# Kernel tuning notes

Hardware: AMD Instinct MI355X
Metric: run time of the kernel (lower is better)

Reference implementation:

```python
import jax, jax.numpy as jnp
import numpy as np

K = 3          # kernel size
PAD = 1        # padding
# deformable conv v2: offset conv (2*K*K ch), modulator conv (K*K ch, 2*sigmoid), main 3x3 conv, ReLU


def _conv2d(x, w, b):
    y = jax.lax.conv_general_dilated(x, w, (1, 1), ((PAD, PAD), (PAD, PAD)),
                                     dimension_numbers=('NCHW', 'OIHW', 'NCHW'))
    return y + b[None, :, None, None]


def _bilinear_gather(x, py, px):
    # x: [B,C,H,W]; py/px: [B,K2,H,W] float sample coords; zero outside image.
    B, C, H, W = x.shape
    y0 = jnp.floor(py)
    x0 = jnp.floor(px)
    wy1 = py - y0
    wx1 = px - x0
    wy0 = 1.0 - wy1
    wx0 = 1.0 - wx1
    xf = x.reshape(B, C, H * W)

    def gather(yi, xi):
        valid = (yi >= 0) & (yi <= H - 1) & (xi >= 0) & (xi <= W - 1)
        yc = jnp.clip(yi, 0, H - 1).astype(jnp.int32)
        xc = jnp.clip(xi, 0, W - 1).astype(jnp.int32)
        idx = (yc * W + xc).reshape(B, -1)                      # [B, K2*H*W]
        v = jax.vmap(lambda xb, ib: xb[:, ib])(xf, idx)         # [B, C, K2*H*W]
        v = v.reshape(B, C, *yi.shape[1:])                      # [B, C, K2, H, W]
        return v * valid[:, None].astype(x.dtype)

    return (gather(y0, x0) * (wy0 * wx0)[:, None]
            + gather(y0, x0 + 1) * (wy0 * wx1)[:, None]
            + gather(y0 + 1, x0) * (wy1 * wx0)[:, None]
            + gather(y0 + 1, x0 + 1) * (wy1 * wx1)[:, None])


def _deform_conv(data, w, b, w_off, b_off, w_mod, b_mod):
    B, Cin, H, W = data.shape
    off = _conv2d(data, w_off, b_off)                           # [B, 2*K2, H, W]
    mask = 2.0 * jax.nn.sigmoid(_conv2d(data, w_mod, b_mod))    # [B, K2, H, W]
    off = off.reshape(B, K * K, 2, H, W)                        # (dy, dx) per tap
    dy, dx = off[:, :, 0], off[:, :, 1]
    ki, kj = jnp.meshgrid(jnp.arange(K), jnp.arange(K), indexing='ij')
    ki = ki.reshape(-1).astype(data.dtype)
    kj = kj.reshape(-1).astype(data.dtype)
    hs = jnp.arange(H, dtype=data.dtype)
    ws = jnp.arange(W, dtype=data.dtype)
    py = hs[None, None, :, None] - PAD + ki[None, :, None, None] + dy
    px = ws[None, None, None, :] - PAD + kj[None, :, None, None] + dx
    sampled = _bilinear_gather(data, py, px)                    # [B, Cin, K2, H, W]
    sampled = sampled * mask[:, None]
    out = jnp.einsum('bckhw,ock->bohw', sampled, w.reshape(w.shape[0], Cin, K * K))
    return out + b[None, :, None, None]


def setup_inputs() -> dict:
    key = jax.random.key(0)
    ks = jax.random.split(key, 7)
    B, Cin, Cout, H, W = 8, 64, 64, 128, 128
    fan = Cin * K * K
    return {
        'data': jax.random.normal(ks[0], (B, Cin, H, W), jnp.float32),
        'w': jax.random.normal(ks[1], (Cout, Cin, K, K), jnp.float32) / np.sqrt(fan),
        'b': jax.random.normal(ks[2], (Cout,), jnp.float32) * 0.01,
        'w_off': jax.random.normal(ks[3], (2 * K * K, Cin, K, K), jnp.float32) * (0.1 / np.sqrt(fan)),
        'b_off': jnp.zeros((2 * K * K,), jnp.float32),
        'w_mod': jax.random.normal(ks[4], (K * K, Cin, K, K), jnp.float32) * (0.1 / np.sqrt(fan)),
        'b_mod': jnp.zeros((K * K,), jnp.float32),
    }


def reference(data, w, b, w_off, b_off, w_mod, b_mod):
    return jax.nn.relu(_deform_conv(data, w, b, w_off, b_off, w_mod, b_mod))
```

## Files before the change

### kernel.cpp

```cpp
#include <hip/hip_runtime.h>
#include <hip/hip_bf16.h>
#include <cstdint>


typedef __attribute__((ext_vector_type(8))) short short8;
typedef __attribute__((ext_vector_type(4))) float floatx4;
typedef __attribute__((ext_vector_type(2))) float floatx2;

__device__ __forceinline__ unsigned short f2bf(float x) {
    unsigned int u = __float_as_uint(x);
    u += 0x7fffu + ((u >> 16) & 1u);
    return (unsigned short)(u >> 16);
}
__device__ __forceinline__ unsigned int pack2bf(float lo, float hi) {
    unsigned int ul = __float_as_uint(lo); ul += 0x7fffu + ((ul >> 16) & 1u);
    unsigned int uh = __float_as_uint(hi); uh += 0x7fffu + ((uh >> 16) & 1u);
    return __builtin_amdgcn_perm(uh, ul, 0x07060302u);
}
__device__ __forceinline__ floatx2 up2(unsigned int u) {
    floatx2 r;
    r.x = __uint_as_float(u << 16);
    r.y = __uint_as_float(u & 0xffff0000u);
    return r;
}
__device__ __forceinline__ unsigned int blend2pk(unsigned int a, unsigned int b,
                                                 unsigned int c, unsigned int d,
                                                 float4 fw) {
    floatx2 s = up2(a) * fw.x;
    s += up2(b) * fw.y;
    s += up2(c) * fw.z;
    s += up2(d) * fw.w;
    __hip_bfloat162 h = __float22bfloat162_rn(make_float2(s.x, s.y));
    return *(unsigned int*)&h;
}

#define OFF_DATAT 0u
#define OFF_OFFP  16777216u
#define OFF_WM    30932992u
#define OFF_W27   31006720u
#define OFF_B27   31043584u

__global__ void pack_weights_k(const float* __restrict__ w,
                               const float* __restrict__ w_off,
                               const float* __restrict__ w_mod,
                               const float* __restrict__ b_off,
                               const float* __restrict__ b_mod,
                               unsigned short* __restrict__ wpackM,
                               unsigned short* __restrict__ wpack27,
                               float* __restrict__ bias27) {
    int t = blockIdx.x * 256 + threadIdx.x;
    if (t < 64 * 576) {
        int o = t / 576, kk = t % 576;
        int k = kk >> 6, c = kk & 63;
        wpackM[t] = f2bf(w[(o * 64 + c) * 9 + k]);
        return;
    }
    t -= 64 * 576;
    if (t < 32 * 576) {
        int o = t / 576, kk = t % 576;
        int k = kk >> 6, c = kk & 63;
        float v = 0.f;
        if (o < 18)      v = w_off[(o * 64 + c) * 9 + k];
        else if (o < 27) v = w_mod[((o - 18) * 64 + c) * 9 + k];
        wpack27[t] = f2bf(v);
        if (kk == 0) bias27[o] = (o < 18) ? b_off[o] : (o < 27 ? b_mod[o - 18] : 0.f);
    }
}

__global__ __launch_bounds__(256) void transpose_k(const float* __restrict__ x,
                                                   unsigned short* __restrict__ xt) {
    __shared__ float tile[64][65];
    int blk  = blockIdx.x;
    int b    = blk >> 8;
    int pos0 = (blk & 255) << 6;
    int lane = threadIdx.x & 63;
    int g    = threadIdx.x >> 6;
    for (int c = g; c < 64; c += 4)
        tile[c][lane] = x[(((b << 6) + c) << 14) + pos0 + lane];
    __syncthreads();
    int c2 = lane & 31;
    for (int i = g; i < 32; i += 4) {
        int pr = (i << 1) + (lane >> 5);
        unsigned int d = pack2bf(tile[c2 << 1][pr], tile[(c2 << 1) + 1][pr]);
        *(unsigned int*)&xt[((size_t)((b << 14) + pos0 + pr) << 6) + (c2 << 1)] = d;
    }
}

__global__ __launch_bounds__(256) void conv27_k(const unsigned short* __restrict__ xt,
                                                const unsigned short* __restrict__ wpack27,
                                                const float* __restrict__ bias27,
                                                float* __restrict__ offP) {
    __shared__ unsigned short tile[4][66][72];
    int blk   = blockIdx.x;
    int b     = blk >> 7;
    int patch = blk & 127;
    int m     = patch >> 1;
    int h     = patch & 1;
    int tid   = threadIdx.x;
    int lane  = tid & 63, wv = tid >> 6;
    int r = lane & 15, q = lane >> 4;

    const unsigned short* xb = xt + ((size_t)b << 20);

    {
        int g = tid >> 3, j = tid & 7;
        #pragma unroll
        for (int rr = 0; rr < 4; ++rr) {
            int sy = (m << 1) + rr - 1;
            #pragma unroll
            for (int ci = 0; ci < 3; ++ci) {
                int col = g + (ci << 5);
                if (col < 66) {
                    int sx = (h << 6) + col - 1;
                    uint4 v = {0u, 0u, 0u, 0u};
                    if (sy >= 0 && sy < 128 && sx >= 0 && sx < 128)
                        v = *(const uint4*)&xb[(size_t)(((sy << 7) + sx) << 6) + (j << 3)];
                    *(uint4*)&tile[rr][col][j << 3] = v;
                }
            }
        }
    }
    __syncthreads();

    floatx4 acc[4] = {};
    #pragma unroll
    for (int k = 0; k < 9; ++k) {
        int ki = k / 3, kj = k % 3;
        #pragma unroll
        for (int ch = 0; ch < 2; ++ch) {
            short8 a0 = *(const short8*)&wpack27[(r)      * 576 + (k << 6) + (ch << 5) + (q << 3)];
            short8 a1 = *(const short8*)&wpack27[(16 + r) * 576 + (k << 6) + (ch << 5) + (q << 3)];
            #pragma unroll
            for (int tr = 0; tr < 2; ++tr) {
                short8 bfrag = *(const short8*)&tile[tr + ki][(wv << 4) + r + kj][(ch << 5) + (q << 3)];
                acc[0 + tr] = __builtin_amdgcn_mfma_f32_16x16x32_bf16(a0, bfrag, acc[0 + tr], 0, 0, 0);
                acc[2 + tr] = __builtin_amdgcn_mfma_f32_16x16x32_bf16(a1, bfrag, acc[2 + tr], 0, 0, 0);
            }
        }
    }

    #pragma unroll
    for (int s = 0; s < 2; ++s) {
        #pragma unroll
        for (int tr = 0; tr < 2; ++tr) {
            #pragma unroll
            for (int reg = 0; reg < 4; ++reg) {
                int oc = (s << 4) + (q << 2) + reg;
                if (oc >= 27) continue;
                int pos = (((m << 1) + tr) << 7) + (h << 6) + (wv << 4) + r;
                float v = acc[(s << 1) + tr][reg] + bias27[oc];
                int kk, comp;
                if (oc < 18) { kk = oc >> 1; comp = oc & 1; }
                else         { kk = oc - 18; comp = 2; v = 2.f / (1.f + __expf(-v)); }
                offP[(size_t)(((b * 9 + kk) * 3 + comp) << 14) + pos] = v;
            }
        }
    }
}

__global__ __launch_bounds__(256) void deform_main_k(const unsigned short* __restrict__ xt,
                                                     const unsigned short* __restrict__ wpackM,
                                                     const float* __restrict__ offP,
                                                     const float* __restrict__ bias,
                                                     float* __restrict__ out) {
    __shared__ int4   pOff[576];
    __shared__ float4 pW[576];
    __shared__ unsigned short samp[2][64][72];
    int blk  = blockIdx.x;
    int b    = blk >> 8;
    int pos0 = (blk & 255) << 6;
    int tid  = threadIdx.x;
    int lane = tid & 63, wv = tid >> 6;
    int r = lane & 15, q = lane >> 4;
    int pg = lane >> 3;
    int j8 = lane & 7;

    const char* xbb = (const char*)(xt + ((size_t)b << 20));

    for (int e = tid; e < 576; e += 256) {
        int k = e >> 6, p = e & 63;
        int pos = pos0 + p;
        const float* offk = offP + ((size_t)((b * 9 + k) * 3) << 14);
        float dy = offk[pos];
        float dx = offk[16384 + pos];
        float m  = offk[32768 + pos];
        float py = (float)(pos >> 7) + (float)(k / 3 - 1) + dy;
        float px = (float)(pos & 127) + (float)(k % 3 - 1) + dx;
        float y0f = floorf(py), x0f = floorf(px);
        int y0 = (int)y0f, x0 = (int)x0f;
        float wy1 = py - y0f, wx1 = px - x0f;
        float wy0 = 1.f - wy1, wx0 = 1.f - wx1;
        bool vy0 = (y0 >= 0) && (y0 < 128);
        bool vy1 = (y0 >= -1) && (y0 < 127);
        bool vx0 = (x0 >= 0) && (x0 < 128);
        bool vx1 = (x0 >= -1) && (x0 < 127);
        float w00 = (vy0 && vx0) ? m * wy0 * wx0 : 0.f;
        float w01 = (vy0 && vx1) ? m * wy0 * wx1 : 0.f;
        float w10 = (vy1 && vx0) ? m * wy1 * wx0 : 0.f;
        float w11 = (vy1 && vx1) ? m * wy1 * wx1 : 0.f;
        int y0c = min(max(y0, 0), 127), y1c = min(max(y0 + 1, 0), 127);
        int x0c = min(max(x0, 0), 127), x1c = min(max(x0 + 1, 0), 127);
        pOff[e] = make_int4(((y0c << 7) + x0c) << 7, ((y0c << 7) + x1c) << 7,
                            ((y1c << 7) + x0c) << 7, ((y1c << 7) + x1c) << 7);
        pW[e] = make_float4(w00, w01, w10, w11);
    }
    __syncthreads();

    floatx4 acc[4] = {};
    const char* xp = xbb + (j8 << 4);
    const unsigned short* wrow = wpackM + ((wv << 4) + r) * 576 + (q << 3);

    uint4  c00[2], c01[2], c10[2], c11[2];
    float4 cw[2];
    short8 afC[2], afN[2];

    auto issue = [&](int k) {
        #pragma unroll
        for (int i = 0; i < 2; ++i) {
            int e  = (k << 6) + (wv << 4) + (i << 3) + pg;
            int4   io = pOff[e];
            cw[i]  = pW[e];
            c00[i] = *(const uint4*)(xp + io.x);
            c01[i] = *(const uint4*)(xp + io.y);
            c10[i] = *(const uint4*)(xp + io.z);
            c11[i] = *(const uint4*)(xp + io.w);
        }
    };
    auto blendStore = [&](int buf) {
        #pragma unroll
        for (int i = 0; i < 2; ++i) {
            int p = (wv << 4) + (i << 3) + pg;
            uint4 o4;
            o4.x = blend2pk(c00[i].x, c01[i].x, c10[i].x, c11[i].x, cw[i]);
            o4.y = blend2pk(c00[i].y, c01[i].y, c10[i].y, c11[i].y, cw[i]);
            o4.z = blend2pk(c00[i].z, c01[i].z, c10[i].z, c11[i].z, cw[i]);
            o4.w = blend2pk(c00[i].w, c01[i].w, c10[i].w, c11[i].w, cw[i]);
            *(uint4*)&samp[buf][p][j8 << 3] = o4;
        }
    };

    issue(0);
    afC[0] = *(const short8*)&wrow[0];
    afC[1] = *(const short8*)&wrow[32];
    blendStore(0);

    for (int k = 0; k < 9; ++k) {
        if (k < 8) {
            issue(k + 1);
            afN[0] = *(const short8*)&wrow[((k + 1) << 6)];
            afN[1] = *(const short8*)&wrow[((k + 1) << 6) + 32];
        }
        __syncthreads();
        #pragma unroll
        for (int ch = 0; ch < 2; ++ch) {
            #pragma unroll
            for (int nt = 0; nt < 4; ++nt) {
                short8 bfrag = *(const short8*)&samp[k & 1][(nt << 4) + r][(ch << 5) + (q << 3)];
                acc[nt] = __builtin_amdgcn_mfma_f32_16x16x32_bf16(afC[ch], bfrag, acc[nt], 0, 0, 0);
            }
        }
        if (k < 8) {
            blendStore((k + 1) & 1);
            afC[0] = afN[0];
            afC[1] = afN[1];
        }
    }

    #pragma unroll
    for (int nt = 0; nt < 4; ++nt) {
        #pragma unroll
        for (int reg = 0; reg < 4; ++reg) {
            int oc  = (wv << 4) + (q << 2) + reg;
            int pos = pos0 + (nt << 4) + r;
            float v = acc[nt][reg] + bias[oc];
            out[(size_t)(((b << 6) + oc) << 14) + pos] = fmaxf(v, 0.f);
        }
    }
}

extern "C" void kernel_launch(void* const* d_in, const int* in_sizes, int n_in,
                              void* d_out, int out_size, void* d_ws, size_t ws_size,
                              hipStream_t stream) {
    const float* data  = (const float*)d_in[0];
    const float* w     = (const float*)d_in[1];
    const float* bias  = (const float*)d_in[2];
    const float* w_off = (const float*)d_in[3];
    const float* b_off = (const float*)d_in[4];
    const float* w_mod = (const float*)d_in[5];
    const float* b_mod = (const float*)d_in[6];
    float* out = (float*)d_out;

    char* ws = (char*)d_ws;
    unsigned short* dataT   = (unsigned short*)(ws + OFF_DATAT);
    float*          offP    = (float*)(ws + OFF_OFFP);
    unsigned short* wpackM  = (unsigned short*)(ws + OFF_WM);
    unsigned short* wpack27 = (unsigned short*)(ws + OFF_W27);
    float*          bias27  = (float*)(ws + OFF_B27);

    pack_weights_k<<<216, 256, 0, stream>>>(w, w_off, w_mod, b_off, b_mod,
                                            wpackM, wpack27, bias27);
    transpose_k<<<2048, 256, 0, stream>>>(data, dataT);
    conv27_k<<<1024, 256, 0, stream>>>(dataT, wpack27, bias27, offP);
    deform_main_k<<<2048, 256, 0, stream>>>(dataT, wpackM, offP, bias, out);
}
```

Baseline: 165.1 us.

## Fuse offset/mask conv into deformable main kernel and merge prep kernels

The offset/modulator 3x3 conv is now computed inside the deformable-conv kernel for each 64-pixel row segment. A 3-row halo is loaded into shared memory and the result is kept in a shared buffer that overlays the halo through a union, so the offP intermediate no longer makes a round trip through global memory. The transpose and weight-packing kernels are merged into a single launch, cutting launches from four to two. The trade-off is that each block reloads a 3-row halo, and the extra shared-memory use and barriers in the fused kernel may lower occupancy.

```diff
diff --git a/kernel.cpp b/kernel.cpp
--- a/kernel.cpp
+++ b/kernel.cpp
@@ -35,20 +35,35 @@
 }
 
 #define OFF_DATAT 0u
-#define OFF_OFFP  16777216u
-#define OFF_WM    30932992u
-#define OFF_W27   31006720u
-#define OFF_B27   31043584u
-
-__global__ void pack_weights_k(const float* __restrict__ w,
-                               const float* __restrict__ w_off,
-                               const float* __restrict__ w_mod,
-                               const float* __restrict__ b_off,
-                               const float* __restrict__ b_mod,
-                               unsigned short* __restrict__ wpackM,
-                               unsigned short* __restrict__ wpack27,
-                               float* __restrict__ bias27) {
-    int t = blockIdx.x * 256 + threadIdx.x;
+#define OFF_WM    16777216u
+#define OFF_W27   16850944u
+
+__global__ __launch_bounds__(256) void prep_k(const float* __restrict__ x,
+                                              unsigned short* __restrict__ xt,
+                                              const float* __restrict__ w,
+                                              const float* __restrict__ w_off,
+                                              const float* __restrict__ w_mod,
+                                              unsigned short* __restrict__ wpackM,
+                                              unsigned short* __restrict__ wpack27) {
+    __shared__ float tile[64][65];
+    int blk = blockIdx.x;
+    if (blk < 2048) {
+        int b    = blk >> 8;
+        int pos0 = (blk & 255) << 6;
+        int lane = threadIdx.x & 63;
+        int g    = threadIdx.x >> 6;
+        for (int c = g; c < 64; c += 4)
+            tile[c][lane] = x[(((b << 6) + c) << 14) + pos0 + lane];
+        __syncthreads();
+        int c2 = lane & 31;
+        for (int i = g; i < 32; i += 4) {
+            int pr = (i << 1) + (lane >> 5);
+            unsigned int d = pack2bf(tile[c2 << 1][pr], tile[(c2 << 1) + 1][pr]);
+            *(unsigned int*)&xt[((size_t)((b << 14) + pos0 + pr) << 6) + (c2 << 1)] = d;
+        }
+        return;
+    }
+    int t = (blk - 2048) * 256 + threadIdx.x;
     if (t < 64 * 576) {
         int o = t / 576, kk = t % 576;
         int k = kk >> 6, c = kk & 63;
@@ -63,50 +78,45 @@
         if (o < 18)      v = w_off[(o * 64 + c) * 9 + k];
         else if (o < 27) v = w_mod[((o - 18) * 64 + c) * 9 + k];
         wpack27[t] = f2bf(v);
-        if (kk == 0) bias27[o] = (o < 18) ? b_off[o] : (o < 27 ? b_mod[o - 18] : 0.f);
-    }
-}
-
-__global__ __launch_bounds__(256) void transpose_k(const float* __restrict__ x,
-                                                   unsigned short* __restrict__ xt) {
-    __shared__ float tile[64][65];
+    }
+}
+
+__global__ __launch_bounds__(256) void deform_fused_k(const unsigned short* __restrict__ xt,
+                                                      const unsigned short* __restrict__ wpackM,
+                                                      const unsigned short* __restrict__ wpack27,
+                                                      const float* __restrict__ b_off,
+                                                      const float* __restrict__ b_mod,
+                                                      const float* __restrict__ bias,
+                                                      float* __restrict__ out) {
+    __shared__ union {
+        unsigned short halo[3][66][72];
+        struct {
+            float convOut[32][64];
+            unsigned short samp[2][64][72];
+        } s2;
+    } U;
+    __shared__ int4   pOff[576];
+    __shared__ float4 pW[576];
+
     int blk  = blockIdx.x;
     int b    = blk >> 8;
     int pos0 = (blk & 255) << 6;
-    int lane = threadIdx.x & 63;
-    int g    = threadIdx.x >> 6;
-    for (int c = g; c < 64; c += 4)
-        tile[c][lane] = x[(((b << 6) + c) << 14) + pos0 + lane];
-    __syncthreads();
-    int c2 = lane & 31;
-    for (int i = g; i < 32; i += 4) {
-        int pr = (i << 1) + (lane >> 5);
-        unsigned int d = pack2bf(tile[c2 << 1][pr], tile[(c2 << 1) + 1][pr]);
-        *(unsigned int*)&xt[((size_t)((b << 14) + pos0 + pr) << 6) + (c2 << 1)] = d;
-    }
-}
-
-__global__ __launch_bounds__(256) void conv27_k(const unsigned short* __restrict__ xt,
-                                                const unsigned short* __restrict__ wpack27,
-                                                const float* __restrict__ bias27,
-                                                float* __restrict__ offP) {
-    __shared__ unsigned short tile[4][66][72];
-    int blk   = blockIdx.x;
-    int b     = blk >> 7;
-    int patch = blk & 127;
-    int m     = patch >> 1;
-    int h     = patch & 1;
-    int tid   = threadIdx.x;
-    int lane  = tid & 63, wv = tid >> 6;
+    int y    = (blk & 255) >> 1;
+    int h    = blk & 1;
+    int tid  = threadIdx.x;
+    int lane = tid & 63, wv = tid >> 6;
     int r = lane & 15, q = lane >> 4;
-
-    const unsigned short* xb = xt + ((size_t)b << 20);
+    int pg = lane >> 3;
+    int j8 = lane & 7;
+
+    const unsigned short* xb  = xt + ((size_t)b << 20);
+    const char*           xbb = (const char*)xb;
 
     {
         int g = tid >> 3, j = tid & 7;
         #pragma unroll
-        for (int rr = 0; rr < 4; ++rr) {
-            int sy = (m << 1) + rr - 1;
+        for (int rr = 0; rr < 3; ++rr) {
+            int sy = y + rr - 1;
             #pragma unroll
             for (int ci = 0; ci < 3; ++ci) {
                 int col = g + (ci << 5);
@@ -115,75 +125,50 @@
                     uint4 v = {0u, 0u, 0u, 0u};
                     if (sy >= 0 && sy < 128 && sx >= 0 && sx < 128)
                         v = *(const uint4*)&xb[(size_t)(((sy << 7) + sx) << 6) + (j << 3)];
-                    *(uint4*)&tile[rr][col][j << 3] = v;
+                    *(uint4*)&U.halo[rr][col][j << 3] = v;
                 }
             }
         }
     }
     __syncthreads();
 
-    floatx4 acc[4] = {};
-    #pragma unroll
-    for (int k = 0; k < 9; ++k) {
-        int ki = k / 3, kj = k % 3;
-        #pragma unroll
-        for (int ch = 0; ch < 2; ++ch) {
-            short8 a0 = *(const short8*)&wpack27[(r)      * 576 + (k << 6) + (ch << 5) + (q << 3)];
-            short8 a1 = *(const short8*)&wpack27[(16 + r) * 576 + (k << 6) + (ch << 5) + (q << 3)];
-            #pragma unroll
-            for (int tr = 0; tr < 2; ++tr) {
-                short8 bfrag = *(const short8*)&tile[tr + ki][(wv << 4) + r + kj][(ch << 5) + (q << 3)];
-                acc[0 + tr] = __builtin_amdgcn_mfma_f32_16x16x32_bf16(a0, bfrag, acc[0 + tr], 0, 0, 0);
-                acc[2 + tr] = __builtin_amdgcn_mfma_f32_16x16x32_bf16(a1, bfrag, acc[2 + tr], 0, 0, 0);
-            }
-        }
-    }
-
-    #pragma unroll
-    for (int s = 0; s < 2; ++s) {
-        #pragma unroll
-        for (int tr = 0; tr < 2; ++tr) {
+    {
+        int i_oc = wv >> 1, j_pos = wv & 1;
+        floatx4 acc2[2] = {};
+        #pragma unroll
+        for (int k = 0; k < 9; ++k) {
+            int ki = k / 3, kj = k % 3;
+            #pragma unroll
+            for (int ch = 0; ch < 2; ++ch) {
+                short8 a = *(const short8*)&wpack27[((i_oc << 4) + r) * 576 + (k << 6) + (ch << 5) + (q << 3)];
+                #pragma unroll
+                for (int nt = 0; nt < 2; ++nt) {
+                    int col = (j_pos << 5) + (nt << 4) + r + kj;
+                    short8 bf = *(const short8*)&U.halo[ki][col][(ch << 5) + (q << 3)];
+                    acc2[nt] = __builtin_amdgcn_mfma_f32_16x16x32_bf16(a, bf, acc2[nt], 0, 0, 0);
+                }
+            }
+        }
+        __syncthreads();
+        #pragma unroll
+        for (int nt = 0; nt < 2; ++nt) {
             #pragma unroll
             for (int reg = 0; reg < 4; ++reg) {
-                int oc = (s << 4) + (q << 2) + reg;
-                if (oc >= 27) continue;
-                int pos = (((m << 1) + tr) << 7) + (h << 6) + (wv << 4) + r;
-                float v = acc[(s << 1) + tr][reg] + bias27[oc];
-                int kk, comp;
-                if (oc < 18) { kk = oc >> 1; comp = oc & 1; }
-                else         { kk = oc - 18; comp = 2; v = 2.f / (1.f + __expf(-v)); }
-                offP[(size_t)(((b * 9 + kk) * 3 + comp) << 14) + pos] = v;
-            }
-        }
-    }
-}
-
-__global__ __launch_bounds__(256) void deform_main_k(const unsigned short* __restrict__ xt,
-                                                     const unsigned short* __restrict__ wpackM,
-                                                     const float* __restrict__ offP,
-                                                     const float* __restrict__ bias,
-                                                     float* __restrict__ out) {
-    __shared__ int4   pOff[576];
-    __shared__ float4 pW[576];
-    __shared__ unsigned short samp[2][64][72];
-    int blk  = blockIdx.x;
-    int b    = blk >> 8;
-    int pos0 = (blk & 255) << 6;
-    int tid  = threadIdx.x;
-    int lane = tid & 63, wv = tid >> 6;
-    int r = lane & 15, q = lane >> 4;
-    int pg = lane >> 3;
-    int j8 = lane & 7;
-
-    const char* xbb = (const char*)(xt + ((size_t)b << 20));
+                int oc  = (i_oc << 4) + (q << 2) + reg;
+                int pl  = (j_pos << 5) + (nt << 4) + r;
+                U.s2.convOut[oc][pl] = acc2[nt][reg];
+            }
+        }
+    }
+    __syncthreads();
 
     for (int e = tid; e < 576; e += 256) {
         int k = e >> 6, p = e & 63;
         int pos = pos0 + p;
-        const float* offk = offP + ((size_t)((b * 9 + k) * 3) << 14);
-        float dy = offk[pos];
-        float dx = offk[16384 + pos];
-        float m  = offk[32768 + pos];
+        float dy = U.s2.convOut[(k << 1)][p]     + b_off[(k << 1)];
+        float dx = U.s2.convOut[(k << 1) + 1][p] + b_off[(k << 1) + 1];
+        float mm = U.s2.convOut[18 + k][p]       + b_mod[k];
+        float m  = 2.f / (1.f + __expf(-mm));
         float py = (float)(pos >> 7) + (float)(k / 3 - 1) + dy;
         float px = (float)(pos & 127) + (float)(k % 3 - 1) + dx;
         float y0f = floorf(py), x0f = floorf(px);
@@ -235,7 +220,7 @@
             o4.y = blend2pk(c00[i].y, c01[i].y, c10[i].y, c11[i].y, cw[i]);
             o4.z = blend2pk(c00[i].z, c01[i].z, c10[i].z, c11[i].z, cw[i]);
             o4.w = blend2pk(c00[i].w, c01[i].w, c10[i].w, c11[i].w, cw[i]);
-            *(uint4*)&samp[buf][p][j8 << 3] = o4;
+            *(uint4*)&U.s2.samp[buf][p][j8 << 3] = o4;
         }
     };
 
@@ -255,7 +240,7 @@
         for (int ch = 0; ch < 2; ++ch) {
             #pragma unroll
             for (int nt = 0; nt < 4; ++nt) {
-                short8 bfrag = *(const short8*)&samp[k & 1][(nt << 4) + r][(ch << 5) + (q << 3)];
+                short8 bfrag = *(const short8*)&U.s2.samp[k & 1][(nt << 4) + r][(ch << 5) + (q << 3)];
                 acc[nt] = __builtin_amdgcn_mfma_f32_16x16x32_bf16(afC[ch], bfrag, acc[nt], 0, 0, 0);
             }
         }
@@ -292,14 +277,10 @@
 
     char* ws = (char*)d_ws;
     unsigned short* dataT   = (unsigned short*)(ws + OFF_DATAT);
-    float*          offP    = (float*)(ws + OFF_OFFP);
     unsigned short* wpackM  = (unsigned short*)(ws + OFF_WM);
     unsigned short* wpack27 = (unsigned short*)(ws + OFF_W27);
-    float*          bias27  = (float*)(ws + OFF_B27);
-
-    pack_weights_k<<<216, 256, 0, stream>>>(w, w_off, w_mod, b_off, b_mod,
-                                            wpackM, wpack27, bias27);
-    transpose_k<<<2048, 256, 0, stream>>>(data, dataT);
-    conv27_k<<<1024, 256, 0, stream>>>(dataT, wpack27, bias27, offP);
-    deform_main_k<<<2048, 256, 0, stream>>>(dataT, wpackM, offP, bias, out);
-}
+
+    prep_k<<<2264, 256, 0, stream>>>(data, dataT, w, w_off, w_mod, wpackM, wpack27);
+    deform_fused_k<<<2048, 256, 0, stream>>>(dataT, wpackM, wpack27,
+                                             b_off, b_mod, bias, out);
+}
```

Result: slower. 178.2 us (+7.9%).

## Sample directly into MFMA B fragments and merge weight packing with transpose

Applied to the files above, without the earlier changes.

The deformable main kernel no longer stages bilinear samples in a double-buffered shared-memory tile with barriers. Each wave now gathers and blends its own 16 pixels straight into MFMA B-operand registers, and loops over all 64 output channels by reading weight A-fragments from global memory every tap. The transpose and weight-packing kernels are also merged into one launch to save a kernel launch. The cost is more global weight loads and less latency hiding, since the prefetching of the next tap's gathers was removed.

```diff
diff --git a/kernel.cpp b/kernel.cpp
--- a/kernel.cpp
+++ b/kernel.cpp
@@ -40,15 +40,35 @@
 #define OFF_W27   31006720u
 #define OFF_B27   31043584u
 
-__global__ void pack_weights_k(const float* __restrict__ w,
-                               const float* __restrict__ w_off,
-                               const float* __restrict__ w_mod,
-                               const float* __restrict__ b_off,
-                               const float* __restrict__ b_mod,
-                               unsigned short* __restrict__ wpackM,
-                               unsigned short* __restrict__ wpack27,
-                               float* __restrict__ bias27) {
-    int t = blockIdx.x * 256 + threadIdx.x;
+__global__ __launch_bounds__(256) void prep_k(const float* __restrict__ x,
+                                              unsigned short* __restrict__ xt,
+                                              const float* __restrict__ w,
+                                              const float* __restrict__ w_off,
+                                              const float* __restrict__ w_mod,
+                                              const float* __restrict__ b_off,
+                                              const float* __restrict__ b_mod,
+                                              unsigned short* __restrict__ wpackM,
+                                              unsigned short* __restrict__ wpack27,
+                                              float* __restrict__ bias27) {
+    __shared__ float tile[64][65];
+    int blk = blockIdx.x;
+    if (blk < 2048) {
+        int b    = blk >> 8;
+        int pos0 = (blk & 255) << 6;
+        int lane = threadIdx.x & 63;
+        int g    = threadIdx.x >> 6;
+        for (int c = g; c < 64; c += 4)
+            tile[c][lane] = x[(((b << 6) + c) << 14) + pos0 + lane];
+        __syncthreads();
+        int c2 = lane & 31;
+        for (int i = g; i < 32; i += 4) {
+            int pr = (i << 1) + (lane >> 5);
+            unsigned int d = pack2bf(tile[c2 << 1][pr], tile[(c2 << 1) + 1][pr]);
+            *(unsigned int*)&xt[((size_t)((b << 14) + pos0 + pr) << 6) + (c2 << 1)] = d;
+        }
+        return;
+    }
+    int t = (blk - 2048) * 256 + threadIdx.x;
     if (t < 64 * 576) {
         int o = t / 576, kk = t % 576;
         int k = kk >> 6, c = kk & 63;
@@ -64,25 +84,6 @@
         else if (o < 27) v = w_mod[((o - 18) * 64 + c) * 9 + k];
         wpack27[t] = f2bf(v);
         if (kk == 0) bias27[o] = (o < 18) ? b_off[o] : (o < 27 ? b_mod[o - 18] : 0.f);
-    }
-}
-
-__global__ __launch_bounds__(256) void transpose_k(const float* __restrict__ x,
-                                                   unsigned short* __restrict__ xt) {
-    __shared__ float tile[64][65];
-    int blk  = blockIdx.x;
-    int b    = blk >> 8;
-    int pos0 = (blk & 255) << 6;
-    int lane = threadIdx.x & 63;
-    int g    = threadIdx.x >> 6;
-    for (int c = g; c < 64; c += 4)
-        tile[c][lane] = x[(((b << 6) + c) << 14) + pos0 + lane];
-    __syncthreads();
-    int c2 = lane & 31;
-    for (int i = g; i < 32; i += 4) {
-        int pr = (i << 1) + (lane >> 5);
-        unsigned int d = pack2bf(tile[c2 << 1][pr], tile[(c2 << 1) + 1][pr]);
-        *(unsigned int*)&xt[((size_t)((b << 14) + pos0 + pr) << 6) + (c2 << 1)] = d;
     }
 }
 
@@ -165,17 +166,12 @@
                                                      float* __restrict__ out) {
     __shared__ int4   pOff[576];
     __shared__ float4 pW[576];
-    __shared__ unsigned short samp[2][64][72];
     int blk  = blockIdx.x;
     int b    = blk >> 8;
     int pos0 = (blk & 255) << 6;
     int tid  = threadIdx.x;
     int lane = tid & 63, wv = tid >> 6;
     int r = lane & 15, q = lane >> 4;
-    int pg = lane >> 3;
-    int j8 = lane & 7;
-
-    const char* xbb = (const char*)(xt + ((size_t)b << 20));
 
     for (int e = tid; e < 576; e += 256) {
         int k = e >> 6, p = e & 63;
@@ -207,72 +203,53 @@
     __syncthreads();
 
     floatx4 acc[4] = {};
-    const char* xp = xbb + (j8 << 4);
-    const unsigned short* wrow = wpackM + ((wv << 4) + r) * 576 + (q << 3);
-
-    uint4  c00[2], c01[2], c10[2], c11[2];
-    float4 cw[2];
-    short8 afC[2], afN[2];
-
-    auto issue = [&](int k) {
-        #pragma unroll
-        for (int i = 0; i < 2; ++i) {
-            int e  = (k << 6) + (wv << 4) + (i << 3) + pg;
-            int4   io = pOff[e];
-            cw[i]  = pW[e];
-            c00[i] = *(const uint4*)(xp + io.x);
-            c01[i] = *(const uint4*)(xp + io.y);
-            c10[i] = *(const uint4*)(xp + io.z);
-            c11[i] = *(const uint4*)(xp + io.w);
-        }
-    };
-    auto blendStore = [&](int buf) {
-        #pragma unroll
-        for (int i = 0; i < 2; ++i) {
-            int p = (wv << 4) + (i << 3) + pg;
+    const char* xq = (const char*)(xt + ((size_t)b << 20)) + (q << 4);
+    const unsigned short* wbase = wpackM + r * 576 + (q << 3);
+
+    int4   io = pOff[(wv << 4) + r];
+    float4 fw = pW[(wv << 4) + r];
+
+    for (int k = 0; k < 9; ++k) {
+        int4 ioN; float4 fwN;
+        if (k < 8) {
+            int eN = ((k + 1) << 6) + (wv << 4) + r;
+            ioN = pOff[eN];
+            fwN = pW[eN];
+        }
+        short8 bfr[2];
+        #pragma unroll
+        for (int ch = 0; ch < 2; ++ch) {
+            const char* base = xq + (ch << 6);
+            uint4 u00 = *(const uint4*)(base + io.x);
+            uint4 u01 = *(const uint4*)(base + io.y);
+            uint4 u10 = *(const uint4*)(base + io.z);
+            uint4 u11 = *(const uint4*)(base + io.w);
             uint4 o4;
-            o4.x = blend2pk(c00[i].x, c01[i].x, c10[i].x, c11[i].x, cw[i]);
-            o4.y = blend2pk(c00[i].y, c01[i].y, c10[i].y, c11[i].y, cw[i]);
-            o4.z = blend2pk(c00[i].z, c01[i].z, c10[i].z, c11[i].z, cw[i]);
-            o4.w = blend2pk(c00[i].w, c01[i].w, c10[i].w, c11[i].w, cw[i]);
-            *(uint4*)&samp[buf][p][j8 << 3] = o4;
-        }
-    };
-
-    issue(0);
-    afC[0] = *(const short8*)&wrow[0];
-    afC[1] = *(const short8*)&wrow[32];
-    blendStore(0);
-
-    for (int k = 0; k < 9; ++k) {
-        if (k < 8) {
-            issue(k + 1);
-            afN[0] = *(const short8*)&wrow[((k + 1) << 6)];
-            afN[1] = *(const short8*)&wrow[((k + 1) << 6) + 32];
-        }
-        __syncthreads();
-        #pragma unroll
-        for (int ch = 0; ch < 2; ++ch) {
-            #pragma unroll
-            for (int nt = 0; nt < 4; ++nt) {
-                short8 bfrag = *(const short8*)&samp[k & 1][(nt << 4) + r][(ch << 5) + (q << 3)];
-                acc[nt] = __builtin_amdgcn_mfma_f32_16x16x32_bf16(afC[ch], bfrag, acc[nt], 0, 0, 0);
-            }
-        }
-        if (k < 8) {
-            blendStore((k + 1) & 1);
-            afC[0] = afN[0];
-            afC[1] = afN[1];
-        }
+            o4.x = blend2pk(u00.x, u01.x, u10.x, u11.x, fw);
+            o4.y = blend2pk(u00.y, u01.y, u10.y, u11.y, fw);
+            o4.z = blend2pk(u00.z, u01.z, u10.z, u11.z, fw);
+            o4.w = blend2pk(u00.w, u01.w, u10.w, u11.w, fw);
+            union { uint4 u; short8 s; } cv; cv.u = o4;
+            bfr[ch] = cv.s;
+        }
+        #pragma unroll
+        for (int st = 0; st < 4; ++st) {
+            #pragma unroll
+            for (int ch = 0; ch < 2; ++ch) {
+                short8 a = *(const short8*)&wbase[(st << 4) * 576 + (k << 6) + (ch << 5)];
+                acc[st] = __builtin_amdgcn_mfma_f32_16x16x32_bf16(a, bfr[ch], acc[st], 0, 0, 0);
+            }
+        }
+        io = ioN; fw = fwN;
     }
 
     #pragma unroll
-    for (int nt = 0; nt < 4; ++nt) {
+    for (int st = 0; st < 4; ++st) {
         #pragma unroll
         for (int reg = 0; reg < 4; ++reg) {
-            int oc  = (wv << 4) + (q << 2) + reg;
-            int pos = pos0 + (nt << 4) + r;
-            float v = acc[nt][reg] + bias[oc];
+            int oc  = (st << 4) + (q << 2) + reg;
+            int pos = pos0 + (wv << 4) + r;
+            float v = acc[st][reg] + bias[oc];
             out[(size_t)(((b << 6) + oc) << 14) + pos] = fmaxf(v, 0.f);
         }
     }
@@ -297,9 +274,8 @@
     unsigned short* wpack27 = (unsigned short*)(ws + OFF_W27);
     float*          bias27  = (float*)(ws + OFF_B27);
 
-    pack_weights_k<<<216, 256, 0, stream>>>(w, w_off, w_mod, b_off, b_mod,
-                                            wpackM, wpack27, bias27);
-    transpose_k<<<2048, 256, 0, stream>>>(data, dataT);
+    prep_k<<<2264, 256, 0, stream>>>(data, dataT, w, w_off, w_mod,
+                                     b_off, b_mod, wpackM, wpack27, bias27);
     conv27_k<<<1024, 256, 0, stream>>>(dataT, wpack27, bias27, offP);
     deform_main_k<<<2048, 256, 0, stream>>>(dataT, wpackM, offP, bias, out);
 }
```

Result: slower. 251.0 us (+52.0%).
